# Performance work log

Hardware: AMD Instinct MI355X
Metric: run time of the kernel (lower is better)

## Reference

```python
import jax, jax.numpy as jnp
import numpy as np

RADIUS = 0.4   # 0.2 * nlayer, nlayer = 2
NSAMPLE = 32   # k


def _fps(xyz, m):
    """Farthest point sampling. xyz: (B, N, 3) -> idx (B, m) int32.
    Matches pointnet2 CUDA kernel: first sampled point is index 0."""
    B, N, _ = xyz.shape

    def step(carry, _):
        dist, far = carry
        centroid = jnp.take_along_axis(xyz, far[:, None, None], axis=1)  # (B,1,3)
        d = jnp.sum((xyz - centroid) ** 2, axis=-1)                      # (B,N)
        dist = jnp.minimum(dist, d)
        return (dist, jnp.argmax(dist, axis=-1).astype(jnp.int32)), far

    init = (jnp.full((B, N), jnp.inf, dtype=xyz.dtype),
            jnp.zeros((B,), dtype=jnp.int32))
    _, idx = jax.lax.scan(step, init, None, length=m)  # (m, B)
    return idx.T                                       # (B, m)


def _ball_query(radius, k, xyz, new_xyz):
    """xyz (B,N,3), new_xyz (B,M,3) -> (B,M,k) int32.
    First k in-radius indices in ascending index order; slots past the
    number of in-radius points are filled with the first found index
    (pointnet2 ball_query semantics)."""
    N = xyz.shape[1]
    d2 = jnp.sum((new_xyz[:, :, None, :] - xyz[:, None, :, :]) ** 2, axis=-1)  # (B,M,N)
    key = jnp.where(d2 < radius * radius,
                    jnp.arange(N, dtype=jnp.int32), jnp.int32(N))              # (B,M,N)
    topv, _ = jax.lax.top_k(-key, k)   # k smallest keys, ascending
    idx = -topv                        # (B,M,k)
    valid = idx < N
    idx = jnp.where(valid, idx, idx[..., :1])  # pad with first found index
    return idx


def _group(t, idx):
    """t (B,C,N), idx (B,M,k) -> (B,C,M,k)."""
    return jnp.take_along_axis(t[:, :, None, :], idx[:, None, :, :], axis=3)


def setup_inputs() -> dict:
    key = jax.random.key(0)
    k1, k2, k3 = jax.random.split(key, 3)
    return {
        "x": jax.random.normal(k1, (8, 3, 8192), dtype=jnp.float32),
        "feature": jax.random.normal(k2, (8, 64, 8192), dtype=jnp.float32),
        "weight": jax.random.normal(k3, (64, 64), dtype=jnp.float32) / 8.0,
        "num_pool": 2048,
    }


def reference(x, feature, weight, num_pool):
    # x: (B,3,N) coordinates, feature: (B,C,N), weight: 1x1 conv (C_out, C_in)
    xyz = jnp.transpose(x, (0, 2, 1))                       # (B,N,3)
    fps_idx = _fps(xyz, num_pool)                           # (B,M)
    new_xyz = jnp.take_along_axis(xyz, fps_idx[:, :, None], axis=1)  # (B,M,3)
    sub_idx = _ball_query(RADIUS, NSAMPLE, xyz, new_xyz)    # (B,M,k)

    x_out = _group(x, sub_idx).max(axis=-1)                 # (B,3,M)
    fg = _group(feature, sub_idx)                           # (B,C,M,k)
    f_out = jnp.einsum('oc,bcmk->bomk', weight, fg).max(axis=-1)  # (B,C,M)
    return x_out, f_out
```

## Files before the change

### kernel.cpp

```cpp
#include <hip/hip_runtime.h>
#include <cstdint>
#include <cstddef>

#define BB 8
#define NN 8192
#define CC 64
#define MM 2048
#define KK 32

typedef float vfloat2 __attribute__((ext_vector_type(2)));

__device__ __forceinline__ float sqdist_exact(float x, float y, float z,
                                              float cx, float cy, float cz) {
    float dx = __fsub_rn(x, cx);
    float dy = __fsub_rn(y, cy);
    float dz = __fsub_rn(z, cz);
    return __fadd_rn(__fadd_rn(__fmul_rn(dx, dx), __fmul_rn(dy, dy)),
                     __fmul_rn(dz, dz));
}

template <int CTRL>
__device__ __forceinline__ unsigned long long dpp_max_u64(unsigned long long key) {
    int lo = (int)(unsigned)key;
    int hi = (int)(unsigned)(key >> 32);
    int slo = __builtin_amdgcn_update_dpp(0, lo, CTRL, 0xF, 0xF, true);
    int shi = __builtin_amdgcn_update_dpp(0, hi, CTRL, 0xF, 0xF, true);
    unsigned long long o = ((unsigned long long)(unsigned)shi << 32) | (unsigned)slo;
    return o > key ? o : key;
}

__device__ __forceinline__ int octile(float v) {
    return (v > -1.1503494f) + (v > -0.6744898f) + (v > -0.3186394f) + (v > 0.0f) +
           (v > 0.3186394f) + (v > 0.6744898f) + (v > 1.1503494f);
}

__device__ __forceinline__ int morton9(int bx, int by, int bz) {
    int m = (bz & 1) | ((bz & 2) << 2) | ((bz & 4) << 4);
    m |= ((by & 1) << 1) | ((by & 2) << 3) | ((by & 4) << 5);
    m |= ((bx & 1) << 2) | ((bx & 2) << 4) | ((bx & 4) << 6);
    return m;
}

__global__ __launch_bounds__(512) void fps_kernel(const float* __restrict__ x,
                                                  int* __restrict__ fps_idx) {
#pragma clang fp contract(off)
    const int b = blockIdx.x;
    const int tid = threadIdx.x;
    const int lane = tid & 63;
    const int wv = tid >> 6;
    const float* xb = x + (size_t)b * 3 * NN;
    int* fps_store = fps_idx + b * MM;

    __shared__ float sx[NN];
    __shared__ float sy[NN];
    __shared__ float sz[NN];
    __shared__ int sidx[NN];
    __shared__ int hist[512];
    __shared__ int scanb[512];
    __shared__ unsigned long long red2[2][8];

    const vfloat2* gx = (const vfloat2*)xb;
    const vfloat2* gy = (const vfloat2*)(xb + NN);
    const vfloat2* gz = (const vfloat2*)(xb + 2 * NN);

    vfloat2 lx[8], ly[8], lz[8];
#pragma unroll
    for (int p = 0; p < 8; ++p) {
        const int e = tid + p * 512;
        lx[p] = gx[e];
        ly[p] = gy[e];
        lz[p] = gz[e];
        ((vfloat2*)sx)[e] = lx[p];
        ((vfloat2*)sy)[e] = ly[p];
        ((vfloat2*)sz)[e] = lz[p];
    }
    hist[tid] = 0;
    __syncthreads();

    int mybin[16];
#pragma unroll
    for (int p = 0; p < 8; ++p) {
        int b0 = morton9(octile(lx[p].x), octile(ly[p].x), octile(lz[p].x));
        int b1 = morton9(octile(lx[p].y), octile(ly[p].y), octile(lz[p].y));
        mybin[2 * p] = b0;
        mybin[2 * p + 1] = b1;
        atomicAdd(&hist[b0], 1);
        atomicAdd(&hist[b1], 1);
    }
    __syncthreads();
    int own = hist[tid];
    scanb[tid] = own;
    __syncthreads();
    for (int off = 1; off < 512; off <<= 1) {
        int add = (tid >= off) ? scanb[tid - off] : 0;
        __syncthreads();
        scanb[tid] += add;
        __syncthreads();
    }
    hist[tid] = scanb[tid] - own;
    __syncthreads();
#pragma unroll
    for (int p = 0; p < 8; ++p) {
        const int i0 = 2 * (tid + p * 512);
        int pos0 = atomicAdd(&hist[mybin[2 * p]], 1);
        sidx[pos0] = i0;
        int pos1 = atomicAdd(&hist[mybin[2 * p + 1]], 1);
        sidx[pos1] = i0 + 1;
    }
    __syncthreads();

    float px[16], py[16], pz[16], dist[16];
    int idxr[16];
#pragma unroll
    for (int p = 0; p < 16; ++p) {
        const int j = sidx[tid * 16 + p];
        idxr[p] = j;
        px[p] = sx[j];
        py[p] = sy[j];
        pz[p] = sz[j];
        dist[p] = INFINITY;
    }
    float blx = px[0], bhx = px[0];
    float bly = py[0], bhy = py[0];
    float blz = pz[0], bhz = pz[0];
#pragma unroll
    for (int p = 1; p < 16; ++p) {
        blx = fminf(blx, px[p]); bhx = fmaxf(bhx, px[p]);
        bly = fminf(bly, py[p]); bhy = fmaxf(bhy, py[p]);
        blz = fminf(blz, pz[p]); bhz = fmaxf(bhz, pz[p]);
    }

    float cmax = INFINITY;
    int cidx = idxr[0];
    int far = 0;
    for (int t = 0; t < MM; ++t) {
        if (tid == 0) fps_store[t] = far;
        const float cx = sx[far];
        const float cy = sy[far];
        const float cz = sz[far];

        float qx = cx - fminf(fmaxf(cx, blx), bhx);
        float qy = cy - fminf(fmaxf(cy, bly), bhy);
        float qz = cz - fminf(fmaxf(cz, blz), bhz);
        float bound = (qx * qx + qy * qy) + qz * qz;
        if (!(bound * 0.999f >= cmax)) {
            float mv = -1.0f;
#pragma unroll
            for (int p = 0; p < 16; ++p) {
                float dx = px[p] - cx;
                float dy = py[p] - cy;
                float dz = pz[p] - cz;
                float s = (dx * dx + dy * dy) + dz * dz;
                float nd = fminf(dist[p], s);
                dist[p] = nd;
                mv = fmaxf(mv, nd);
            }
            int mi = 0x7FFFFFFF;
#pragma unroll
            for (int p = 0; p < 16; ++p) {
                int cand = (dist[p] == mv) ? idxr[p] : 0x7FFFFFFF;
                mi = min(mi, cand);
            }
            cmax = mv;
            cidx = mi;
        }
        unsigned long long key =
            ((unsigned long long)__float_as_uint(cmax) << 32) | (unsigned)(~(unsigned)cidx);
        key = dpp_max_u64<0x111>(key);
        key = dpp_max_u64<0x112>(key);
        key = dpp_max_u64<0x114>(key);
        key = dpp_max_u64<0x118>(key);
        key = dpp_max_u64<0x142>(key);
        key = dpp_max_u64<0x143>(key);
        if (lane == 63) red2[t & 1][wv] = key;
        __syncthreads();
        unsigned long long best = red2[t & 1][0];
#pragma unroll
        for (int j = 1; j < 8; ++j) {
            unsigned long long o2 = red2[t & 1][j];
            if (o2 > best) best = o2;
        }
        far = (int)(~(unsigned)best);
    }
}

__global__ __launch_bounds__(256) void transform_kernel(const float* __restrict__ feature,
                                                        const float* __restrict__ weight,
                                                        float* __restrict__ g) {
    __shared__ float Wl[64 * 64];
    const int tid = threadIdx.x;
    for (int k = tid; k < 64 * 64; k += 256) Wl[k] = weight[k];
    __syncthreads();

    const int P = blockIdx.x * 256 + tid;
    const int b = P >> 13;
    const int n = P & (NN - 1);
    const float* fb = feature + (size_t)b * CC * NN + n;

    float fr[64];
#pragma unroll
    for (int c = 0; c < 64; ++c) fr[c] = fb[(size_t)c * NN];

    float* go = g + ((size_t)b << 19) + (size_t)n * 64;
    for (int o = 0; o < 64; o += 4) {
        const float* w0 = &Wl[o * 64];
        const float* w1 = w0 + 64;
        const float* w2 = w0 + 128;
        const float* w3 = w0 + 192;
        float a0 = 0.f, a1 = 0.f, a2 = 0.f, a3 = 0.f;
#pragma unroll
        for (int c = 0; c < 64; c += 4) {
            float4 v0 = *(const float4*)(w0 + c);
            float4 v1 = *(const float4*)(w1 + c);
            float4 v2 = *(const float4*)(w2 + c);
            float4 v3 = *(const float4*)(w3 + c);
            a0 += v0.x * fr[c] + v0.y * fr[c + 1] + v0.z * fr[c + 2] + v0.w * fr[c + 3];
            a1 += v1.x * fr[c] + v1.y * fr[c + 1] + v1.z * fr[c + 2] + v1.w * fr[c + 3];
            a2 += v2.x * fr[c] + v2.y * fr[c + 1] + v2.z * fr[c + 2] + v2.w * fr[c + 3];
            a3 += v3.x * fr[c] + v3.y * fr[c + 1] + v3.z * fr[c + 2] + v3.w * fr[c + 3];
        }
        float4 r;
        r.x = a0; r.y = a1; r.z = a2; r.w = a3;
        *(float4*)(go + o) = r;
    }
}

__global__ __launch_bounds__(256) void bq_kernel(const float* __restrict__ x,
                                                 const int* __restrict__ fps_idx,
                                                 int* __restrict__ sub_idx,
                                                 float* __restrict__ xout) {
    const float R2 = (float)(0.4 * 0.4);
    int gw = (int)((blockIdx.x * 256 + threadIdx.x) >> 6);
    const int lane = threadIdx.x & 63;
    gw = __builtin_amdgcn_readfirstlane(gw);
    const int b = gw >> 11;
    const int m = gw & (MM - 1);
    const float* xb = x + (size_t)b * 3 * NN;

    const int ctr = fps_idx[gw];
    const float cx = xb[ctr];
    const float cy = xb[NN + ctr];
    const float cz = xb[2 * NN + ctr];

    int* sid = sub_idx + (size_t)gw * KK;
    int found = 0;
    int first = 0;
    float mx = -INFINITY, my = -INFINITY, mz = -INFINITY;

    for (int base = 0; base < NN; base += 64) {
        const int i = base + lane;
        const float xx = xb[i];
        const float yy = xb[NN + i];
        const float zz = xb[2 * NN + i];
        const float d2 = sqdist_exact(xx, yy, zz, cx, cy, cz);
        const bool q = d2 < R2;
        const unsigned long long mask = __ballot(q);
        if (q) {
            int pos = found + (int)__popcll(mask & ((1ull << lane) - 1ull));
            if (pos < KK) {
                sid[pos] = i;
                mx = fmaxf(mx, xx);
                my = fmaxf(my, yy);
                mz = fmaxf(mz, zz);
            }
        }
        if (found == 0 && mask != 0ull) first = base + (int)__builtin_ctzll(mask);
        found += (int)__popcll(mask);
        if (found >= KK) break;
    }
    if (found < KK) {
        if (lane < KK - found) sid[found + lane] = first;
    }
#pragma unroll
    for (int off = 32; off >= 1; off >>= 1) {
        mx = fmaxf(mx, __shfl_xor(mx, off, 64));
        my = fmaxf(my, __shfl_xor(my, off, 64));
        mz = fmaxf(mz, __shfl_xor(mz, off, 64));
    }
    if (lane == 0) {
        xout[(size_t)b * 3 * MM + 0 * MM + m] = mx;
        xout[(size_t)b * 3 * MM + 1 * MM + m] = my;
        xout[(size_t)b * 3 * MM + 2 * MM + m] = mz;
    }
}

__global__ __launch_bounds__(256) void gather_kernel(const float* __restrict__ g,
                                                     const int* __restrict__ sub_idx,
                                                     float* __restrict__ fout) {
    int gw = (int)((blockIdx.x * 256 + threadIdx.x) >> 6);
    const int lane = threadIdx.x & 63;
    gw = __builtin_amdgcn_readfirstlane(gw);
    const int b = gw >> 11;
    const int m = gw & (MM - 1);
    const int* sid = sub_idx + (size_t)gw * KK;
    const float* gb = g + ((size_t)b << 19);
    float acc = -INFINITY;
#pragma unroll
    for (int j = 0; j < KK; ++j) {
        const int id = sid[j];
        acc = fmaxf(acc, gb[(size_t)id * 64 + lane]);
    }
    fout[((size_t)b << 17) + ((size_t)lane << 11) + m] = acc;
}

extern "C" void kernel_launch(void* const* d_in, const int* in_sizes, int n_in,
                              void* d_out, int out_size, void* d_ws, size_t ws_size,
                              hipStream_t stream) {
    const float* x = (const float*)d_in[0];
    const float* feature = (const float*)d_in[1];
    const float* weight = (const float*)d_in[2];

    float* out = (float*)d_out;
    float* xout = out;
    float* fout = out + BB * 3 * MM;

    char* ws = (char*)d_ws;
    int* fps_idx = (int*)ws;
    int* sub_idx = (int*)(ws + (size_t)BB * MM * 4);
    float* g = (float*)(ws + (size_t)BB * MM * 4 + (size_t)BB * MM * KK * 4);

    fps_kernel<<<BB, 512, 0, stream>>>(x, fps_idx);
    transform_kernel<<<(BB * NN) / 256, 256, 0, stream>>>(feature, weight, g);
    bq_kernel<<<(BB * MM * 64) / 256, 256, 0, stream>>>(x, fps_idx, sub_idx, xout);
    gather_kernel<<<(BB * MM * 64) / 256, 256, 0, stream>>>(g, sub_idx, fout);
}
```

Baseline: 2.021 ms.

## Split FPS wave argmax into 32-bit max/min DPP passes and buffer indices in LDS

Replaces the 64-bit packed-key DPP max reduction in the farthest-point-sampling loop with a 32-bit max over distances, a readlane broadcast, and a 32-bit min over the indices that hit the max. The cross-wave max over the eight partial keys becomes a balanced tree instead of a serial chain. Sampled indices are kept in a shared buffer and written to global memory once after the loop, so thread 0 no longer issues a global store every iteration. The serial per-iteration latency is the target. The cost is a second DPP chain and a readlane per step, plus 8KB more LDS.

```diff
diff --git a/kernel.cpp b/kernel.cpp
--- a/kernel.cpp
+++ b/kernel.cpp
@@ -20,13 +20,14 @@
 }
 
 template <int CTRL>
-__device__ __forceinline__ unsigned long long dpp_max_u64(unsigned long long key) {
-    int lo = (int)(unsigned)key;
-    int hi = (int)(unsigned)(key >> 32);
-    int slo = __builtin_amdgcn_update_dpp(0, lo, CTRL, 0xF, 0xF, true);
-    int shi = __builtin_amdgcn_update_dpp(0, hi, CTRL, 0xF, 0xF, true);
-    unsigned long long o = ((unsigned long long)(unsigned)shi << 32) | (unsigned)slo;
-    return o > key ? o : key;
+__device__ __forceinline__ unsigned dpp_max_u32(unsigned v) {
+    unsigned s = (unsigned)__builtin_amdgcn_update_dpp(0, (int)v, CTRL, 0xF, 0xF, true);
+    return v > s ? v : s;
+}
+template <int CTRL>
+__device__ __forceinline__ unsigned dpp_min_u32(unsigned v) {
+    unsigned s = (unsigned)__builtin_amdgcn_update_dpp(0x7FFFFFFF, (int)v, CTRL, 0xF, 0xF, false);
+    return v < s ? v : s;
 }
 
 __device__ __forceinline__ int octile(float v) {
@@ -57,6 +58,7 @@
     __shared__ int sidx[NN];
     __shared__ int hist[512];
     __shared__ int scanb[512];
+    __shared__ int sfps[MM];
     __shared__ unsigned long long red2[2][8];
 
     const vfloat2* gx = (const vfloat2*)xb;
@@ -134,7 +136,7 @@
     int cidx = idxr[0];
     int far = 0;
     for (int t = 0; t < MM; ++t) {
-        if (tid == 0) fps_store[t] = far;
+        if (tid == 0) sfps[t] = far;
         const float cx = sx[far];
         const float cy = sy[far];
         const float cz = sz[far];
@@ -164,24 +166,41 @@
             cmax = mv;
             cidx = mi;
         }
-        unsigned long long key =
-            ((unsigned long long)__float_as_uint(cmax) << 32) | (unsigned)(~(unsigned)cidx);
-        key = dpp_max_u64<0x111>(key);
-        key = dpp_max_u64<0x112>(key);
-        key = dpp_max_u64<0x114>(key);
-        key = dpp_max_u64<0x118>(key);
-        key = dpp_max_u64<0x142>(key);
-        key = dpp_max_u64<0x143>(key);
-        if (lane == 63) red2[t & 1][wv] = key;
+
+        unsigned mvb = __float_as_uint(cmax);
+        mvb = dpp_max_u32<0x111>(mvb);
+        mvb = dpp_max_u32<0x112>(mvb);
+        mvb = dpp_max_u32<0x114>(mvb);
+        mvb = dpp_max_u32<0x118>(mvb);
+        mvb = dpp_max_u32<0x142>(mvb);
+        mvb = dpp_max_u32<0x143>(mvb);
+        const unsigned wmax = (unsigned)__builtin_amdgcn_readlane((int)mvb, 63);
+        unsigned midx = (__float_as_uint(cmax) == wmax) ? (unsigned)cidx : 0x7FFFFFFFu;
+        midx = dpp_min_u32<0x111>(midx);
+        midx = dpp_min_u32<0x112>(midx);
+        midx = dpp_min_u32<0x114>(midx);
+        midx = dpp_min_u32<0x118>(midx);
+        midx = dpp_min_u32<0x142>(midx);
+        midx = dpp_min_u32<0x143>(midx);
+        if (lane == 63) {
+            red2[t & 1][wv] =
+                ((unsigned long long)wmax << 32) | (unsigned)(~midx);
+        }
         __syncthreads();
-        unsigned long long best = red2[t & 1][0];
-#pragma unroll
-        for (int j = 1; j < 8; ++j) {
-            unsigned long long o2 = red2[t & 1][j];
-            if (o2 > best) best = o2;
-        }
+        const unsigned long long* r = red2[t & 1];
+        unsigned long long k0 = r[0], k1 = r[1], k2 = r[2], k3 = r[3];
+        unsigned long long k4 = r[4], k5 = r[5], k6 = r[6], k7 = r[7];
+        unsigned long long a0 = k0 > k1 ? k0 : k1;
+        unsigned long long a1 = k2 > k3 ? k2 : k3;
+        unsigned long long a2 = k4 > k5 ? k4 : k5;
+        unsigned long long a3 = k6 > k7 ? k6 : k7;
+        unsigned long long b0 = a0 > a1 ? a0 : a1;
+        unsigned long long b1 = a2 > a3 ? a2 : a3;
+        unsigned long long best = b0 > b1 ? b0 : b1;
         far = (int)(~(unsigned)best);
     }
+    __syncthreads();
+    for (int t = tid; t < MM; t += 512) fps_store[t] = sfps[t];
 }
 
 __global__ __launch_bounds__(256) void transform_kernel(const float* __restrict__ feature,
```

Result: faster. 1.933 ms (-4.4%).
